# Kernel optimization log

Hardware: AMD Instinct MI355X
Metric: run time of the kernel (lower is better)

Reference implementation:

```python
import jax, jax.numpy as jnp
import numpy as np

B, S, D, H, HD = 8, 1374, 384, 6, 64
NUM_PATCHES = 1369  # (518 // 14) ** 2
NUM_PREFIX = 5      # 1 cls + 4 registers


def setup_inputs() -> dict:
    key = jax.random.key(0)
    ks = jax.random.split(key, 10)
    init = 0.02  # truncated_normal(0.02) approximated by scaled normal
    x = jax.random.normal(ks[0], (B, S, D), jnp.float32)
    wq = jax.random.truncated_normal(ks[1], -2.0, 2.0, (D, H, HD), jnp.float32) * init
    wk = jax.random.truncated_normal(ks[2], -2.0, 2.0, (D, H, HD), jnp.float32) * init
    wv = jax.random.truncated_normal(ks[3], -2.0, 2.0, (D, H, HD), jnp.float32) * init
    wo = jax.random.truncated_normal(ks[4], -2.0, 2.0, (H, HD, D), jnp.float32) * init
    bq = jnp.zeros((H, HD), jnp.float32)
    bk = jnp.zeros((H, HD), jnp.float32)
    bv = jnp.zeros((H, HD), jnp.float32)
    bo = jnp.zeros((D,), jnp.float32)
    keep_patch_indices = jax.random.randint(ks[5], (B, NUM_PATCHES), 0, NUM_PATCHES).astype(jnp.int64)
    return {"x": x, "wq": wq, "bq": bq, "wk": wk, "bk": bk, "wv": wv, "bv": bv,
            "wo": wo, "bo": bo, "keep_patch_indices": keep_patch_indices, "k_patches": 685}


def reference(x, wq, bq, wk, bk, wv, bv, wo, bo, keep_patch_indices, k_patches):
    # q/k/v projections: DenseGeneral to (heads, head_dim)
    q = jnp.einsum('bsd,dhe->bshe', x, wq) + bq
    k = jnp.einsum('bsd,dhe->bshe', x, wk) + bk
    v = jnp.einsum('bsd,dhe->bshe', x, wv) + bv

    z = jnp.einsum('bqhd,bkhd->bhqk', q / (HD ** 0.5), k)  # [B,H,S,S]
    attn_logits = z  # saved BEFORE masking (used by 'mse' criterion)

    # dynamic scatter mask: patch columns >= k_patches get -inf
    num_selected = keep_patch_indices.shape[1]
    patch_idx = jnp.arange(num_selected)
    indices_to_mask = jnp.where(patch_idx >= k_patches, patch_idx, num_selected) + NUM_PREFIX
    # out-of-bounds indices (== num_selected + NUM_PREFIX) are dropped by JAX scatter semantics
    z = z.at[:, :, :, indices_to_mask].set(-jnp.inf)

    attn_map = jax.nn.softmax(z, axis=-1)
    zo = jnp.einsum('bhqk,bkhd->bqhd', attn_map, v)
    output = jnp.einsum('bqhd,hdo->bqo', zo, wo) + bo  # wo contracts (heads, head_dim)

    # attn_aggregate = ['cls_token','reg_token','patch_token'], zoom_map_criterion='mse'
    am = attn_logits.mean(axis=1)  # mean over heads -> [B,S,S]
    aggs = jnp.stack([
        am[:, 0:1, :].mean(axis=1),      # cls token
        am[:, 1:5, :].mean(axis=1),      # register tokens
        am[:, 5:1374, :].mean(axis=1),   # patch tokens
    ], axis=1)                            # [B,3,S]
    attn_agg = aggs.mean(axis=1)          # [B,S]
    return output, attn_agg
```

## Files before the change

### kernel.cpp

```cpp
#include <hip/hip_runtime.h>
#include <stdint.h>

#define BB 8
#define SS 1374
#define DD 384
#define HH 6
#define HDIM 64
#define MROWS (BB*SS)
#define NPFX 5
#define SPAD 1376

typedef __attribute__((ext_vector_type(8))) short bf16x8;
typedef __attribute__((ext_vector_type(4))) float f32x4;
typedef __attribute__((ext_vector_type(2))) unsigned int u32x2;
typedef __attribute__((ext_vector_type(4))) unsigned int u32x4;
typedef u32x4 __attribute__((aligned(4))) u32x4_u;

__device__ __forceinline__ unsigned short f2bf(float f){
  union { float f; unsigned int u; } v; v.f = f;
  return (unsigned short)((v.u + 0x7FFFu + ((v.u >> 16) & 1u)) >> 16);
}
__device__ __forceinline__ float bf2f(unsigned short b){
  union { float f; unsigned int u; } v; v.u = ((unsigned int)b) << 16; return v.f;
}
__device__ __forceinline__ unsigned int pk_bf16(float a, float b){
#if __has_builtin(__builtin_amdgcn_cvt_pk_bf16_f32)
  typedef __attribute__((ext_vector_type(2))) __bf16 bfv2;
  bfv2 p = __builtin_amdgcn_cvt_pk_bf16_f32(a, b);
  union { bfv2 v; unsigned int u; } c; c.v = p; return c.u;
#else
  return (unsigned int)f2bf(a) | ((unsigned int)f2bf(b) << 16);
#endif
}

__global__ void k_prep_x(const float* __restrict__ x, unsigned short* __restrict__ xb,
                         float* __restrict__ xbar){
  int b = blockIdx.x / 43, ch = blockIdx.x % 43;
  int d = threadIdx.x;
  int s0 = ch*32, s1 = s0 + 32; if (s1 > SS) s1 = SS;
  float acc = 0.f;
  for (int s = s0; s < s1; ++s){
    float v = x[((size_t)b*SS + s)*DD + d];
    float w = (s == 0) ? (1.f/3.f) : (s < 5) ? (1.f/12.f) : (1.f/4107.f);
    acc += w * v;
    xb[((size_t)b*SS + s)*DD + d] = f2bf(v);
  }
  atomicAdd(&xbar[b*DD + d], acc);
}

__global__ void k_conv_w(const float* __restrict__ wq, const float* __restrict__ wk,
                         const float* __restrict__ wv, const float* __restrict__ wo,
                         unsigned short* __restrict__ wbT, unsigned short* __restrict__ woT){
  int i = blockIdx.x*blockDim.x + threadIdx.x;
  if (i < 1152*384){
    int n = i / 384, d = i % 384;
    const float* w = (n < 384) ? wq : (n < 768) ? wk : wv;
    wbT[i] = f2bf(w[(size_t)d*384 + (n % 384)]);
  } else if (i < 1152*384 + 384*384){
    int j = i - 1152*384;
    int n = j / 384, k = j % 384;
    woT[j] = f2bf(wo[(size_t)k*384 + n]);
  }
}

__global__ void k_qbar(const float* __restrict__ xbar, const float* __restrict__ wq,
                       const float* __restrict__ bq, float* __restrict__ qbar){
  __shared__ float xs[DD];
  int b = blockIdx.x, t = threadIdx.x;
  xs[t] = xbar[b*DD + t];
  __syncthreads();
  float acc = bq[t];
  for (int d = 0; d < DD; ++d) acc += xs[d]*wq[(size_t)d*384 + t];
  qbar[b*384 + t] = acc;
}

__global__ void k_agg(const float* __restrict__ qbar, const unsigned short* __restrict__ kg,
                      float* __restrict__ out_agg){
  __shared__ float qs[384];
  int b = blockIdx.x / 6, sb = blockIdx.x % 6;
  int t = threadIdx.x;
  for (int i = t; i < 384; i += 256) qs[i] = qbar[b*384 + i];
  __syncthreads();
  int s = sb*256 + t;
  if (s >= SS) return;
  float acc = 0.f;
  for (int h = 0; h < HH; ++h){
    const unsigned short* kr = kg + (((size_t)(b*HH + h))*SS + s)*64;
    const float* qh = qs + h*64;
    for (int c = 0; c < 8; ++c){
      u32x4 v = *(const u32x4*)(kr + c*8);
      #pragma unroll
      for (int j = 0; j < 4; ++j){
        unsigned int u = v[j];
        acc += qh[c*8 + 2*j]     * bf2f((unsigned short)(u & 0xFFFFu));
        acc += qh[c*8 + 2*j + 1] * bf2f((unsigned short)(u >> 16));
      }
    }
  }
  out_agg[b*SS + s] = acc * (1.f/48.f);
}

template<int MODE>
__global__ __launch_bounds__(256) void k_gemm(
    const unsigned short* __restrict__ A, const unsigned short* __restrict__ Bt,
    const float* __restrict__ b0, const float* __restrict__ b1, const float* __restrict__ b2,
    unsigned short* __restrict__ qg, unsigned short* __restrict__ kgp,
    unsigned short* __restrict__ vt, float* __restrict__ out)
{
  int mt = blockIdx.x % 86, nt = blockIdx.x / 86;
  const int t = threadIdx.x;
  const int w = t >> 6, lane = t & 63, quad = lane >> 4, l16 = lane & 15;
  const int wm = w >> 1, wn = w & 1;
  constexpr int SMEM_SH = (MODE==0) ? 13824 : 17408;
  __shared__ unsigned short smem[SMEM_SH];
  unsigned short* As = smem;
  unsigned short* Bs = smem + 9216;
  f32x4 acc[4][2];
  #pragma unroll
  for (int i=0;i<4;i++){ acc[i][0] = (f32x4){0,0,0,0}; acc[i][1] = (f32x4){0,0,0,0}; }
  const int m0 = mt*128, n0 = nt*64;

  const int ar = t >> 1, akb = (t & 1) * 32;
  int ga = m0 + ar; if (ga > MROWS-1) ga = MROWS-1;
  const unsigned short* ap = A + (size_t)ga*384 + akb;
  const int br = t >> 2, bkb = (t & 3) * 16;
  const unsigned short* bp = Bt + (size_t)(n0 + br)*384 + bkb;

  u32x4 ra[4], rb[2];
  #pragma unroll
  for (int i=0;i<4;i++) ra[i] = *(const u32x4*)(ap + i*8);
  rb[0] = *(const u32x4*)(bp); rb[1] = *(const u32x4*)(bp + 8);

  for (int kc = 0; kc < 6; ++kc){
    __syncthreads();
    #pragma unroll
    for (int i=0;i<4;i++) *(u32x4*)(As + ar*72 + akb + i*8) = ra[i];
    *(u32x4*)(Bs + br*72 + bkb)     = rb[0];
    *(u32x4*)(Bs + br*72 + bkb + 8) = rb[1];
    __syncthreads();
    if (kc + 1 < 6){
      int kn = (kc+1)*64;
      #pragma unroll
      for (int i=0;i<4;i++) ra[i] = *(const u32x4*)(ap + kn + i*8);
      rb[0] = *(const u32x4*)(bp + kn); rb[1] = *(const u32x4*)(bp + kn + 8);
    }
    #pragma unroll
    for (int kh = 0; kh < 2; ++kh){
      bf16x8 af[4], bfr[2];
      #pragma unroll
      for (int rf = 0; rf < 4; ++rf)
        af[rf] = *(const bf16x8*)(As + (wm*64 + rf*16 + l16)*72 + kh*32 + quad*8);
      #pragma unroll
      for (int cf = 0; cf < 2; ++cf)
        bfr[cf] = *(const bf16x8*)(Bs + (wn*32 + cf*16 + l16)*72 + kh*32 + quad*8);
      #pragma unroll
      for (int rf = 0; rf < 4; ++rf)
        #pragma unroll
        for (int cf = 0; cf < 2; ++cf)
          acc[rf][cf] = __builtin_amdgcn_mfma_f32_16x16x32_bf16(af[rf], bfr[cf], acc[rf][cf], 0,0,0);
    }
  }

  const int b0r = m0 / SS, s0r = m0 % SS;
  __syncthreads();
  if (MODE == 1){
    float* CsF = (float*)smem;
    #pragma unroll
    for (int cf = 0; cf < 2; ++cf){
      int e = wn*32 + cf*16 + l16;
      float bias = b0[n0 + e];
      #pragma unroll
      for (int rf = 0; rf < 4; ++rf){
        int rr = wm*64 + rf*16 + quad*4;
        #pragma unroll
        for (int r4 = 0; r4 < 4; ++r4)
          CsF[(rr + r4)*68 + e] = acc[rf][cf][r4] + bias;
      }
    }
    __syncthreads();
    #pragma unroll
    for (int p = 0; p < 8; ++p){
      int r = p*16 + (t >> 4), c = t & 15;
      int rr = m0 + r;
      if (rr < MROWS){
        f32x4 v = *(const f32x4*)(CsF + r*68 + c*4);
        *(f32x4*)(out + (size_t)rr*384 + n0 + c*4) = v;
      }
    }
  } else {
    const int mat = nt / 6, h = nt - mat*6;
    const float* bvp = (mat==0) ? b0 : (mat==1) ? b1 : b2;
    const float vsc = (mat==0) ? 0.125f : 1.f;
    if (mat < 2){
      unsigned short* Cs = As;
      unsigned short* dst = (mat==0) ? qg : kgp;
      #pragma unroll
      for (int cf = 0; cf < 2; ++cf){
        int e = wn*32 + cf*16 + l16;
        float bias = bvp[h*64 + e];
        #pragma unroll
        for (int rf = 0; rf < 4; ++rf){
          int rr = wm*64 + rf*16 + quad*4;
          #pragma unroll
          for (int r4 = 0; r4 < 4; ++r4)
            Cs[(rr + r4)*72 + e] = f2bf((acc[rf][cf][r4] + bias)*vsc);
        }
      }
      __syncthreads();
      #pragma unroll
      for (int p = 0; p < 4; ++p){
        int r = p*32 + (t >> 3), c = t & 7;
        int rr = m0 + r;
        if (rr < MROWS){
          int s = s0r + r, bb = b0r;
          if (s >= SS){ s -= SS; ++bb; }
          u32x4 v = *(const u32x4*)(Cs + r*72 + c*8);
          *(u32x4*)(dst + (((size_t)(bb*HH + h))*SS + s)*64 + c*8) = v;
        }
      }
    } else {
      unsigned short* CsV = As;
      #pragma unroll
      for (int cf = 0; cf < 2; ++cf){
        int e = wn*32 + cf*16 + l16;
        float bias = bvp[h*64 + e];
        #pragma unroll
        for (int rf = 0; rf < 4; ++rf){
          int rr = wm*64 + rf*16 + quad*4;
          #pragma unroll
          for (int p = 0; p < 2; ++p)
            *(unsigned int*)(CsV + e*136 + rr + p*2) =
                pk_bf16(acc[rf][cf][p*2] + bias, acc[rf][cf][p*2+1] + bias);
        }
      }
      __syncthreads();
      const bool nowrap = (s0r + 127 < SS) && (m0 + 127 < MROWS);
      if (nowrap){
        int e = t >> 2;
        unsigned short* vrow = vt + ((size_t)(b0r*HH + h)*64 + e)*SPAD + s0r;
        #pragma unroll
        for (int i = 0; i < 4; ++i){
          int c = (t & 3)*4 + i;
          u32x4 v = *(const u32x4*)(CsV + e*136 + c*8);
          *(u32x4_u*)(vrow + c*8) = v;
        }
      } else {
        for (int idx = t; idx < 64*64; idx += 256){
          int e = idx >> 6, sp = (idx & 63)*2;
          int rr = m0 + sp;
          if (rr < MROWS){
            int s = s0r + sp, bb = b0r;
            if (s >= SS){ s -= SS; ++bb; }
            *(unsigned int*)(vt + ((size_t)(bb*HH + h)*64 + e)*SPAD + s) =
                *(const unsigned int*)(CsV + e*136 + sp);
          }
        }
      }
    }
  }
}

__global__ __launch_bounds__(256) void k_attn(
    const unsigned short* __restrict__ qg, const unsigned short* __restrict__ kg,
    const unsigned short* __restrict__ vt, unsigned short* __restrict__ zo,
    const int* __restrict__ kpat)
{
  int t = threadIdx.x, w = t >> 6, lane = t & 63, quad = lane >> 4, l16 = lane & 15;
  int wid = blockIdx.x*4 + w;
  int bh = wid / 43, qt = wid - bh*43;
  int q0 = qt*32;
  int SK = NPFX + kpat[0]; if (SK > SS) SK = SS; if (SK < 1) SK = 1;
  int niter = (SK + 63) >> 6;
  __shared__ unsigned short Ps[4][32*72];
  unsigned short* Pw = &Ps[w][0];
  const unsigned short* kbase = kg + ((size_t)bh*SS)*64;
  const unsigned short* vbase = vt + ((size_t)bh*64)*SPAD;

  bf16x8 aq[2][2];
  #pragma unroll
  for (int qf = 0; qf < 2; ++qf){
    int qrow = q0 + qf*16 + l16; if (qrow > SS-1) qrow = SS-1;
    const unsigned short* p = qg + ((size_t)bh*SS + qrow)*64;
    aq[qf][0] = *(const bf16x8*)(p + quad*8);
    aq[qf][1] = *(const bf16x8*)(p + 32 + quad*8);
  }
  f32x4 o[2][4];
  #pragma unroll
  for (int qf=0;qf<2;qf++)
    #pragma unroll
    for (int nc=0;nc<4;nc++) o[qf][nc] = (f32x4){0.f,0.f,0.f,0.f};
  float rsum[2][4] = {{0.f,0.f,0.f,0.f},{0.f,0.f,0.f,0.f}};

  for (int it = 0; it < niter; ++it){
    int k0 = it*64;
    bool tail = (k0 + 64 > SK);
    #pragma unroll
    for (int ks = 0; ks < 2; ++ks){
      bf16x8 kf[2][2];
      #pragma unroll
      for (int ns = 0; ns < 2; ++ns){
        const unsigned short* kr = kbase + (size_t)(k0 + ks*32 + 2*l16 + ns)*64;
        kf[ns][0] = *(const bf16x8*)(kr + quad*8);
        kf[ns][1] = *(const bf16x8*)(kr + 32 + quad*8);
      }
      #pragma unroll
      for (int qf = 0; qf < 2; ++qf){
        float pp[2][4];
        #pragma unroll
        for (int ns = 0; ns < 2; ++ns){
          f32x4 zf = (f32x4){0.f,0.f,0.f,0.f};
          zf = __builtin_amdgcn_mfma_f32_16x16x32_bf16(aq[qf][0], kf[ns][0], zf, 0,0,0);
          zf = __builtin_amdgcn_mfma_f32_16x16x32_bf16(aq[qf][1], kf[ns][1], zf, 0,0,0);
          bool valid = !tail || (k0 + ks*32 + 2*l16 + ns) < SK;
          #pragma unroll
          for (int rg = 0; rg < 4; ++rg) pp[ns][rg] = valid ? __expf(zf[rg]) : 0.f;
        }
        #pragma unroll
        for (int rg = 0; rg < 4; ++rg){
          rsum[qf][rg] += pp[0][rg] + pp[1][rg];
          *(unsigned int*)(Pw + (qf*16 + quad*4 + rg)*72 + ks*32 + 2*l16) =
              pk_bf16(pp[0][rg], pp[1][rg]);
        }
      }
    }
    #pragma unroll
    for (int kc = 0; kc < 2; ++kc){
      bf16x8 ap0 = *(const bf16x8*)(Pw + l16*72        + kc*32 + quad*8);
      bf16x8 ap1 = *(const bf16x8*)(Pw + (16 + l16)*72 + kc*32 + quad*8);
      #pragma unroll
      for (int nc = 0; nc < 4; ++nc){
        bf16x8 vf = *(const bf16x8*)(vbase + (size_t)(nc*16 + l16)*SPAD + k0 + kc*32 + quad*8);
        o[0][nc] = __builtin_amdgcn_mfma_f32_16x16x32_bf16(ap0, vf, o[0][nc], 0,0,0);
        o[1][nc] = __builtin_amdgcn_mfma_f32_16x16x32_bf16(ap1, vf, o[1][nc], 0,0,0);
      }
    }
  }
  int b = bh / HH, h = bh - (bh/HH)*HH;
  #pragma unroll
  for (int qf = 0; qf < 2; ++qf){
    #pragma unroll
    for (int rg = 0; rg < 4; ++rg){
      float s = rsum[qf][rg];
      #pragma unroll
      for (int off = 8; off >= 1; off >>= 1) s += __shfl_xor(s, off);
      int q = q0 + qf*16 + quad*4 + rg;
      if (q >= SS) continue;
      float inv = 1.f / s;
      unsigned short* dst = zo + ((size_t)b*SS + q)*384 + h*64;
      #pragma unroll
      for (int nc = 0; nc < 4; ++nc) dst[nc*16 + l16] = f2bf(o[qf][nc][rg]*inv);
    }
  }
}

extern "C" void kernel_launch(void* const* d_in, const int* in_sizes, int n_in,
                              void* d_out, int out_size, void* d_ws, size_t ws_size,
                              hipStream_t stream){
  const float* x  = (const float*)d_in[0];
  const float* wq = (const float*)d_in[1];
  const float* bq = (const float*)d_in[2];
  const float* wk = (const float*)d_in[3];
  const float* bk = (const float*)d_in[4];
  const float* wv = (const float*)d_in[5];
  const float* bv = (const float*)d_in[6];
  const float* wo = (const float*)d_in[7];
  const float* bo = (const float*)d_in[8];
  const int* kpat = (const int*)d_in[10];
  float* out = (float*)d_out;
  float* out_agg = out + (size_t)MROWS*DD;

  char* ws = (char*)d_ws;
  unsigned short* xb  = (unsigned short*)(ws);
  unsigned short* wbT = (unsigned short*)(ws +  8441856);
  unsigned short* woT = (unsigned short*)(ws +  9326592);
  unsigned short* qg  = (unsigned short*)(ws +  9621504);
  unsigned short* kg  = (unsigned short*)(ws + 18063360);
  unsigned short* vt  = (unsigned short*)(ws + 26505216);
  unsigned short* zo  = (unsigned short*)(ws + 34959360);
  float* xbar         = (float*)(ws + 43401216);
  float* qbar         = (float*)(ws + 43413504);
  (void)in_sizes; (void)n_in; (void)out_size; (void)ws_size;

  hipMemsetAsync(xbar, 0, BB*DD*sizeof(float), stream);
  k_prep_x<<<BB*43, DD, 0, stream>>>(x, xb, xbar);
  k_conv_w<<<((1152*384 + 384*384) + 255)/256, 256, 0, stream>>>(wq, wk, wv, wo, wbT, woT);
  k_qbar<<<BB, DD, 0, stream>>>(xbar, wq, bq, qbar);
  k_gemm<0><<<86*18, 256, 0, stream>>>(xb, wbT, bq, bk, bv, qg, kg, vt, nullptr);
  k_attn<<<516, 256, 0, stream>>>(qg, kg, vt, zo, kpat);
  k_agg<<<BB*6, 256, 0, stream>>>(qbar, kg, out_agg);
  k_gemm<1><<<86*6, 256, 0, stream>>>(zo, woT, bo, nullptr, nullptr, nullptr, nullptr, nullptr, out);
}
```

Before: 208.8 us.

## Software-pipeline K/V loads in attention kernel and halve block size

The attention loop now double-buffers K fragments in registers, prefetching the next 64-key tile's K while the current one is computed, and loads all V fragments at the start of each iteration, ahead of the softmax/P work. Block size drops from 4 to 2 waves with twice as many blocks, which spreads the 2064 wave tasks over more CUs. The aim is to hide global-load latency behind MFMA and exp work. The cost is higher register pressure from the extra K and V buffers, which may lower occupancy.

```diff
diff --git a/kernel.cpp b/kernel.cpp
--- a/kernel.cpp
+++ b/kernel.cpp
@@ -260,18 +260,18 @@
   }
 }
 
-__global__ __launch_bounds__(256) void k_attn(
+__global__ __launch_bounds__(128) void k_attn(
     const unsigned short* __restrict__ qg, const unsigned short* __restrict__ kg,
     const unsigned short* __restrict__ vt, unsigned short* __restrict__ zo,
     const int* __restrict__ kpat)
 {
   int t = threadIdx.x, w = t >> 6, lane = t & 63, quad = lane >> 4, l16 = lane & 15;
-  int wid = blockIdx.x*4 + w;
+  int wid = blockIdx.x*2 + w;
   int bh = wid / 43, qt = wid - bh*43;
   int q0 = qt*32;
   int SK = NPFX + kpat[0]; if (SK > SS) SK = SS; if (SK < 1) SK = 1;
   int niter = (SK + 63) >> 6;
-  __shared__ unsigned short Ps[4][32*72];
+  __shared__ unsigned short Ps[2][32*72];
   unsigned short* Pw = &Ps[w][0];
   const unsigned short* kbase = kg + ((size_t)bh*SS)*64;
   const unsigned short* vbase = vt + ((size_t)bh*64)*SPAD;
@@ -291,26 +291,37 @@
     for (int nc=0;nc<4;nc++) o[qf][nc] = (f32x4){0.f,0.f,0.f,0.f};
   float rsum[2][4] = {{0.f,0.f,0.f,0.f},{0.f,0.f,0.f,0.f}};
 
-  for (int it = 0; it < niter; ++it){
-    int k0 = it*64;
-    bool tail = (k0 + 64 > SK);
-    #pragma unroll
-    for (int ks = 0; ks < 2; ++ks){
-      bf16x8 kf[2][2];
+  auto loadK = [&](int k0, bf16x8 (&kf)[2][2][2]){
+    #pragma unroll
+    for (int ks = 0; ks < 2; ++ks)
       #pragma unroll
       for (int ns = 0; ns < 2; ++ns){
         const unsigned short* kr = kbase + (size_t)(k0 + ks*32 + 2*l16 + ns)*64;
-        kf[ns][0] = *(const bf16x8*)(kr + quad*8);
-        kf[ns][1] = *(const bf16x8*)(kr + 32 + quad*8);
-      }
+        kf[ks][ns][0] = *(const bf16x8*)(kr + quad*8);
+        kf[ks][ns][1] = *(const bf16x8*)(kr + 32 + quad*8);
+      }
+  };
+
+  auto body = [&](int it, bf16x8 (&kfC)[2][2][2], bf16x8 (&kfN)[2][2][2]){
+    int k0 = it*64;
+    bf16x8 vf[2][4];
+    #pragma unroll
+    for (int kc = 0; kc < 2; ++kc)
+      #pragma unroll
+      for (int nc = 0; nc < 4; ++nc)
+        vf[kc][nc] = *(const bf16x8*)(vbase + (size_t)(nc*16 + l16)*SPAD + k0 + kc*32 + quad*8);
+    if (it + 1 < niter) loadK(k0 + 64, kfN);
+    bool tail = (k0 + 64 > SK);
+    #pragma unroll
+    for (int ks = 0; ks < 2; ++ks){
       #pragma unroll
       for (int qf = 0; qf < 2; ++qf){
         float pp[2][4];
         #pragma unroll
         for (int ns = 0; ns < 2; ++ns){
           f32x4 zf = (f32x4){0.f,0.f,0.f,0.f};
-          zf = __builtin_amdgcn_mfma_f32_16x16x32_bf16(aq[qf][0], kf[ns][0], zf, 0,0,0);
-          zf = __builtin_amdgcn_mfma_f32_16x16x32_bf16(aq[qf][1], kf[ns][1], zf, 0,0,0);
+          zf = __builtin_amdgcn_mfma_f32_16x16x32_bf16(aq[qf][0], kfC[ks][ns][0], zf, 0,0,0);
+          zf = __builtin_amdgcn_mfma_f32_16x16x32_bf16(aq[qf][1], kfC[ks][ns][1], zf, 0,0,0);
           bool valid = !tail || (k0 + ks*32 + 2*l16 + ns) < SK;
           #pragma unroll
           for (int rg = 0; rg < 4; ++rg) pp[ns][rg] = valid ? __expf(zf[rg]) : 0.f;
@@ -329,12 +340,19 @@
       bf16x8 ap1 = *(const bf16x8*)(Pw + (16 + l16)*72 + kc*32 + quad*8);
       #pragma unroll
       for (int nc = 0; nc < 4; ++nc){
-        bf16x8 vf = *(const bf16x8*)(vbase + (size_t)(nc*16 + l16)*SPAD + k0 + kc*32 + quad*8);
-        o[0][nc] = __builtin_amdgcn_mfma_f32_16x16x32_bf16(ap0, vf, o[0][nc], 0,0,0);
-        o[1][nc] = __builtin_amdgcn_mfma_f32_16x16x32_bf16(ap1, vf, o[1][nc], 0,0,0);
-      }
-    }
-  }
+        o[0][nc] = __builtin_amdgcn_mfma_f32_16x16x32_bf16(ap0, vf[kc][nc], o[0][nc], 0,0,0);
+        o[1][nc] = __builtin_amdgcn_mfma_f32_16x16x32_bf16(ap1, vf[kc][nc], o[1][nc], 0,0,0);
+      }
+    }
+  };
+
+  bf16x8 kfA[2][2][2], kfB[2][2][2];
+  loadK(0, kfA);
+  for (int it = 0; it < niter; it += 2){
+    body(it, kfA, kfB);
+    if (it + 1 < niter) body(it + 1, kfB, kfA);
+  }
+
   int b = bh / HH, h = bh - (bh/HH)*HH;
   #pragma unroll
   for (int qf = 0; qf < 2; ++qf){
@@ -386,7 +404,7 @@
   k_conv_w<<<((1152*384 + 384*384) + 255)/256, 256, 0, stream>>>(wq, wk, wv, wo, wbT, woT);
   k_qbar<<<BB, DD, 0, stream>>>(xbar, wq, bq, qbar);
   k_gemm<0><<<86*18, 256, 0, stream>>>(xb, wbT, bq, bk, bv, qg, kg, vt, nullptr);
-  k_attn<<<516, 256, 0, stream>>>(qg, kg, vt, zo, kpat);
+  k_attn<<<1032, 128, 0, stream>>>(qg, kg, vt, zo, kpat);
   k_agg<<<BB*6, 256, 0, stream>>>(qbar, kg, out_agg);
   k_gemm<1><<<86*6, 256, 0, stream>>>(zo, woT, bo, nullptr, nullptr, nullptr, nullptr, nullptr, out);
 }
```

After: 198.3 us. 1.05x faster.

## Stage K/V tiles in shared memory with register prefetch in attention kernel

Applied to the files above, without the earlier changes.

The attention kernel now uses 128-thread blocks of two waves, each owning 16 query rows. The block cooperatively loads each 64-key K and V tile into LDS, with the next tile prefetched into registers while the current one is computed. Before, each wave read K and V straight from global memory. The goal is to share K/V loads across waves and hide global latency with more, smaller blocks. The cost is two barriers per iteration and less query reuse per wave: 16 rows instead of 32.

```diff
diff --git a/kernel.cpp b/kernel.cpp
--- a/kernel.cpp
+++ b/kernel.cpp
@@ -260,96 +260,106 @@
   }
 }
 
-__global__ __launch_bounds__(256) void k_attn(
+#define KSTR 72
+__global__ __launch_bounds__(128) void k_attn(
     const unsigned short* __restrict__ qg, const unsigned short* __restrict__ kg,
     const unsigned short* __restrict__ vt, unsigned short* __restrict__ zo,
     const int* __restrict__ kpat)
 {
+  const int QB = 43;
+  int qb = blockIdx.x % QB, bh = blockIdx.x / QB;
   int t = threadIdx.x, w = t >> 6, lane = t & 63, quad = lane >> 4, l16 = lane & 15;
-  int wid = blockIdx.x*4 + w;
-  int bh = wid / 43, qt = wid - bh*43;
-  int q0 = qt*32;
   int SK = NPFX + kpat[0]; if (SK > SS) SK = SS; if (SK < 1) SK = 1;
   int niter = (SK + 63) >> 6;
-  __shared__ unsigned short Ps[4][32*72];
+  __shared__ unsigned short Ks[64*KSTR];
+  __shared__ unsigned short Vs[64*KSTR];
+  __shared__ unsigned short Ps[2][16*KSTR];
   unsigned short* Pw = &Ps[w][0];
+  int q0 = qb*32 + w*16;
+  bf16x8 aq[2];
+  {
+    int qrow = q0 + l16; if (qrow > SS-1) qrow = SS-1;
+    const unsigned short* p = qg + ((size_t)bh*SS + qrow)*64;
+    aq[0] = *(const bf16x8*)(p + quad*8);
+    aq[1] = *(const bf16x8*)(p + 32 + quad*8);
+  }
+  f32x4 o[4];
+  #pragma unroll
+  for (int i=0;i<4;i++) o[i] = (f32x4){0.f,0.f,0.f,0.f};
+  float rsum[4] = {0.f,0.f,0.f,0.f};
+
+  const int srow = t >> 1, shalf = (t & 1)*32;
   const unsigned short* kbase = kg + ((size_t)bh*SS)*64;
   const unsigned short* vbase = vt + ((size_t)bh*64)*SPAD;
-
-  bf16x8 aq[2][2];
+  u32x4 rk[4], rv[4];
   #pragma unroll
-  for (int qf = 0; qf < 2; ++qf){
-    int qrow = q0 + qf*16 + l16; if (qrow > SS-1) qrow = SS-1;
-    const unsigned short* p = qg + ((size_t)bh*SS + qrow)*64;
-    aq[qf][0] = *(const bf16x8*)(p + quad*8);
-    aq[qf][1] = *(const bf16x8*)(p + 32 + quad*8);
-  }
-  f32x4 o[2][4];
-  #pragma unroll
-  for (int qf=0;qf<2;qf++)
-    #pragma unroll
-    for (int nc=0;nc<4;nc++) o[qf][nc] = (f32x4){0.f,0.f,0.f,0.f};
-  float rsum[2][4] = {{0.f,0.f,0.f,0.f},{0.f,0.f,0.f,0.f}};
+  for (int i=0;i<4;i++){
+    rk[i] = *(const u32x4*)(kbase + (size_t)srow*64 + shalf + i*8);
+    rv[i] = *(const u32x4*)(vbase + (size_t)srow*SPAD + shalf + i*8);
+  }
 
   for (int it = 0; it < niter; ++it){
     int k0 = it*64;
+    __syncthreads();
+    #pragma unroll
+    for (int i=0;i<4;i++){
+      *(u32x4*)(Ks + srow*KSTR + shalf + i*8) = rk[i];
+      *(u32x4*)(Vs + srow*KSTR + shalf + i*8) = rv[i];
+    }
+    __syncthreads();
+    if (it + 1 < niter){
+      int kn = k0 + 64;
+      #pragma unroll
+      for (int i=0;i<4;i++){
+        rk[i] = *(const u32x4*)(kbase + (size_t)(kn + srow)*64 + shalf + i*8);
+        rv[i] = *(const u32x4*)(vbase + (size_t)srow*SPAD + kn + shalf + i*8);
+      }
+    }
     bool tail = (k0 + 64 > SK);
     #pragma unroll
     for (int ks = 0; ks < 2; ++ks){
-      bf16x8 kf[2][2];
+      float pp[2][4];
       #pragma unroll
       for (int ns = 0; ns < 2; ++ns){
-        const unsigned short* kr = kbase + (size_t)(k0 + ks*32 + 2*l16 + ns)*64;
-        kf[ns][0] = *(const bf16x8*)(kr + quad*8);
-        kf[ns][1] = *(const bf16x8*)(kr + 32 + quad*8);
-      }
-      #pragma unroll
-      for (int qf = 0; qf < 2; ++qf){
-        float pp[2][4];
-        #pragma unroll
-        for (int ns = 0; ns < 2; ++ns){
-          f32x4 zf = (f32x4){0.f,0.f,0.f,0.f};
-          zf = __builtin_amdgcn_mfma_f32_16x16x32_bf16(aq[qf][0], kf[ns][0], zf, 0,0,0);
-          zf = __builtin_amdgcn_mfma_f32_16x16x32_bf16(aq[qf][1], kf[ns][1], zf, 0,0,0);
-          bool valid = !tail || (k0 + ks*32 + 2*l16 + ns) < SK;
-          #pragma unroll
-          for (int rg = 0; rg < 4; ++rg) pp[ns][rg] = valid ? __expf(zf[rg]) : 0.f;
-        }
-        #pragma unroll
-        for (int rg = 0; rg < 4; ++rg){
-          rsum[qf][rg] += pp[0][rg] + pp[1][rg];
-          *(unsigned int*)(Pw + (qf*16 + quad*4 + rg)*72 + ks*32 + 2*l16) =
-              pk_bf16(pp[0][rg], pp[1][rg]);
-        }
+        f32x4 zf = (f32x4){0.f,0.f,0.f,0.f};
+        #pragma unroll
+        for (int ec = 0; ec < 2; ++ec){
+          bf16x8 bkf = *(const bf16x8*)(Ks + (ks*32 + 2*l16 + ns)*KSTR + ec*32 + quad*8);
+          zf = __builtin_amdgcn_mfma_f32_16x16x32_bf16(aq[ec], bkf, zf, 0,0,0);
+        }
+        bool valid = !tail || (k0 + ks*32 + 2*l16 + ns) < SK;
+        #pragma unroll
+        for (int rg = 0; rg < 4; ++rg) pp[ns][rg] = valid ? __expf(zf[rg]) : 0.f;
+      }
+      #pragma unroll
+      for (int rg = 0; rg < 4; ++rg){
+        rsum[rg] += pp[0][rg] + pp[1][rg];
+        *(unsigned int*)(Pw + (quad*4 + rg)*KSTR + ks*32 + 2*l16) =
+            pk_bf16(pp[0][rg], pp[1][rg]);
       }
     }
     #pragma unroll
     for (int kc = 0; kc < 2; ++kc){
-      bf16x8 ap0 = *(const bf16x8*)(Pw + l16*72        + kc*32 + quad*8);
-      bf16x8 ap1 = *(const bf16x8*)(Pw + (16 + l16)*72 + kc*32 + quad*8);
+      bf16x8 ap = *(const bf16x8*)(Pw + l16*KSTR + kc*32 + quad*8);
       #pragma unroll
       for (int nc = 0; nc < 4; ++nc){
-        bf16x8 vf = *(const bf16x8*)(vbase + (size_t)(nc*16 + l16)*SPAD + k0 + kc*32 + quad*8);
-        o[0][nc] = __builtin_amdgcn_mfma_f32_16x16x32_bf16(ap0, vf, o[0][nc], 0,0,0);
-        o[1][nc] = __builtin_amdgcn_mfma_f32_16x16x32_bf16(ap1, vf, o[1][nc], 0,0,0);
+        bf16x8 vf = *(const bf16x8*)(Vs + (nc*16 + l16)*KSTR + kc*32 + quad*8);
+        o[nc] = __builtin_amdgcn_mfma_f32_16x16x32_bf16(ap, vf, o[nc], 0,0,0);
       }
     }
   }
   int b = bh / HH, h = bh - (bh/HH)*HH;
   #pragma unroll
-  for (int qf = 0; qf < 2; ++qf){
-    #pragma unroll
-    for (int rg = 0; rg < 4; ++rg){
-      float s = rsum[qf][rg];
-      #pragma unroll
-      for (int off = 8; off >= 1; off >>= 1) s += __shfl_xor(s, off);
-      int q = q0 + qf*16 + quad*4 + rg;
-      if (q >= SS) continue;
-      float inv = 1.f / s;
-      unsigned short* dst = zo + ((size_t)b*SS + q)*384 + h*64;
-      #pragma unroll
-      for (int nc = 0; nc < 4; ++nc) dst[nc*16 + l16] = f2bf(o[qf][nc][rg]*inv);
-    }
+  for (int rg = 0; rg < 4; ++rg){
+    float s = rsum[rg];
+    #pragma unroll
+    for (int off = 8; off >= 1; off >>= 1) s += __shfl_xor(s, off);
+    int q = q0 + quad*4 + rg;
+    if (q >= SS) continue;
+    float inv = 1.f / s;
+    unsigned short* dst = zo + ((size_t)b*SS + q)*384 + h*64;
+    #pragma unroll
+    for (int nc = 0; nc < 4; ++nc) dst[nc*16 + l16] = f2bf(o[nc][rg]*inv);
   }
 }
 
@@ -386,7 +396,7 @@
   k_conv_w<<<((1152*384 + 384*384) + 255)/256, 256, 0, stream>>>(wq, wk, wv, wo, wbT, woT);
   k_qbar<<<BB, DD, 0, stream>>>(xbar, wq, bq, qbar);
   k_gemm<0><<<86*18, 256, 0, stream>>>(xb, wbT, bq, bk, bv, qg, kg, vt, nullptr);
-  k_attn<<<516, 256, 0, stream>>>(qg, kg, vt, zo, kpat);
+  k_attn<<<48*43, 128, 0, stream>>>(qg, kg, vt, zo, kpat);
   k_agg<<<BB*6, 256, 0, stream>>>(qbar, kg, out_agg);
   k_gemm<1><<<86*6, 256, 0, stream>>>(zo, woT, bo, nullptr, nullptr, nullptr, nullptr, nullptr, out);
 }
```

New measurement: 191.6 us. 1.09x faster.

## Keep attention probabilities in registers via transposed MFMA, prefetch K tiles

Applied to the files above, without the earlier changes.

Computes S^T = K·Q^T with MFMA so each lane's probability outputs already sit in the B-operand layout for the P·V MFMA. This removes the per-wave LDS round trip for P. It also double-buffers K fragments across 32-key iterations and writes the output as packed vector stores. Register pressure rises from the two K buffers and the V fragments held per iteration.

```diff
diff --git a/kernel.cpp b/kernel.cpp
--- a/kernel.cpp
+++ b/kernel.cpp
@@ -270,9 +270,7 @@
   int bh = wid / 43, qt = wid - bh*43;
   int q0 = qt*32;
   int SK = NPFX + kpat[0]; if (SK > SS) SK = SS; if (SK < 1) SK = 1;
-  int niter = (SK + 63) >> 6;
-  __shared__ unsigned short Ps[4][32*72];
-  unsigned short* Pw = &Ps[w][0];
+  int niter = (SK + 31) >> 5;
   const unsigned short* kbase = kg + ((size_t)bh*SS)*64;
   const unsigned short* vbase = vt + ((size_t)bh*64)*SPAD;
 
@@ -289,66 +287,81 @@
   for (int qf=0;qf<2;qf++)
     #pragma unroll
     for (int nc=0;nc<4;nc++) o[qf][nc] = (f32x4){0.f,0.f,0.f,0.f};
-  float rsum[2][4] = {{0.f,0.f,0.f,0.f},{0.f,0.f,0.f,0.f}};
-
-  for (int it = 0; it < niter; ++it){
-    int k0 = it*64;
-    bool tail = (k0 + 64 > SK);
-    #pragma unroll
-    for (int ks = 0; ks < 2; ++ks){
-      bf16x8 kf[2][2];
-      #pragma unroll
-      for (int ns = 0; ns < 2; ++ns){
-        const unsigned short* kr = kbase + (size_t)(k0 + ks*32 + 2*l16 + ns)*64;
-        kf[ns][0] = *(const bf16x8*)(kr + quad*8);
-        kf[ns][1] = *(const bf16x8*)(kr + 32 + quad*8);
-      }
-      #pragma unroll
-      for (int qf = 0; qf < 2; ++qf){
-        float pp[2][4];
-        #pragma unroll
-        for (int ns = 0; ns < 2; ++ns){
-          f32x4 zf = (f32x4){0.f,0.f,0.f,0.f};
-          zf = __builtin_amdgcn_mfma_f32_16x16x32_bf16(aq[qf][0], kf[ns][0], zf, 0,0,0);
-          zf = __builtin_amdgcn_mfma_f32_16x16x32_bf16(aq[qf][1], kf[ns][1], zf, 0,0,0);
-          bool valid = !tail || (k0 + ks*32 + 2*l16 + ns) < SK;
-          #pragma unroll
-          for (int rg = 0; rg < 4; ++rg) pp[ns][rg] = valid ? __expf(zf[rg]) : 0.f;
-        }
+  float rsum[2] = {0.f, 0.f};
+
+  const int krow_off = ((l16 >> 2) << 3) + (l16 & 3);
+  auto loadK = [&](int k0, bf16x8 (&kf)[2][2]){
+    #pragma unroll
+    for (int s = 0; s < 2; ++s){
+      const unsigned short* kr = kbase + (size_t)(k0 + krow_off + s*4)*64;
+      kf[s][0] = *(const bf16x8*)(kr + quad*8);
+      kf[s][1] = *(const bf16x8*)(kr + 32 + quad*8);
+    }
+  };
+
+  auto body = [&](int it, bf16x8 (&kfC)[2][2], bf16x8 (&kfN)[2][2]){
+    int k0 = it*32;
+    bf16x8 vf[4];
+    #pragma unroll
+    for (int nc = 0; nc < 4; ++nc)
+      vf[nc] = *(const bf16x8*)(vbase + (size_t)(nc*16 + l16)*SPAD + k0 + quad*8);
+    if (it + 1 < niter) loadK(k0 + 32, kfN);
+    bool tail = (k0 + 32 > SK);
+    int kidx0 = k0 + quad*8;
+    float ps[2][2][4];
+    #pragma unroll
+    for (int qf = 0; qf < 2; ++qf){
+      #pragma unroll
+      for (int s = 0; s < 2; ++s){
+        f32x4 zf = (f32x4){0.f,0.f,0.f,0.f};
+        zf = __builtin_amdgcn_mfma_f32_16x16x32_bf16(kfC[s][0], aq[qf][0], zf, 0,0,0);
+        zf = __builtin_amdgcn_mfma_f32_16x16x32_bf16(kfC[s][1], aq[qf][1], zf, 0,0,0);
         #pragma unroll
         for (int rg = 0; rg < 4; ++rg){
-          rsum[qf][rg] += pp[0][rg] + pp[1][rg];
-          *(unsigned int*)(Pw + (qf*16 + quad*4 + rg)*72 + ks*32 + 2*l16) =
-              pk_bf16(pp[0][rg], pp[1][rg]);
-        }
-      }
-    }
-    #pragma unroll
-    for (int kc = 0; kc < 2; ++kc){
-      bf16x8 ap0 = *(const bf16x8*)(Pw + l16*72        + kc*32 + quad*8);
-      bf16x8 ap1 = *(const bf16x8*)(Pw + (16 + l16)*72 + kc*32 + quad*8);
-      #pragma unroll
-      for (int nc = 0; nc < 4; ++nc){
-        bf16x8 vf = *(const bf16x8*)(vbase + (size_t)(nc*16 + l16)*SPAD + k0 + kc*32 + quad*8);
-        o[0][nc] = __builtin_amdgcn_mfma_f32_16x16x32_bf16(ap0, vf, o[0][nc], 0,0,0);
-        o[1][nc] = __builtin_amdgcn_mfma_f32_16x16x32_bf16(ap1, vf, o[1][nc], 0,0,0);
-      }
-    }
-  }
+          bool valid = !tail || (kidx0 + s*4 + rg) < SK;
+          float p = valid ? __expf(zf[rg]) : 0.f;
+          ps[qf][s][rg] = p;
+          rsum[qf] += p;
+        }
+      }
+    }
+    #pragma unroll
+    for (int qf = 0; qf < 2; ++qf){
+      u32x4 pu;
+      pu[0] = pk_bf16(ps[qf][0][0], ps[qf][0][1]);
+      pu[1] = pk_bf16(ps[qf][0][2], ps[qf][0][3]);
+      pu[2] = pk_bf16(ps[qf][1][0], ps[qf][1][1]);
+      pu[3] = pk_bf16(ps[qf][1][2], ps[qf][1][3]);
+      union { u32x4 u; bf16x8 b; } cv; cv.u = pu;
+      #pragma unroll
+      for (int nc = 0; nc < 4; ++nc)
+        o[qf][nc] = __builtin_amdgcn_mfma_f32_16x16x32_bf16(vf[nc], cv.b, o[qf][nc], 0,0,0);
+    }
+  };
+
+  bf16x8 kfA[2][2], kfB[2][2];
+  loadK(0, kfA);
+  for (int it = 0; it < niter; it += 2){
+    body(it, kfA, kfB);
+    if (it + 1 < niter) body(it + 1, kfB, kfA);
+  }
+
   int b = bh / HH, h = bh - (bh/HH)*HH;
   #pragma unroll
   for (int qf = 0; qf < 2; ++qf){
-    #pragma unroll
-    for (int rg = 0; rg < 4; ++rg){
-      float s = rsum[qf][rg];
-      #pragma unroll
-      for (int off = 8; off >= 1; off >>= 1) s += __shfl_xor(s, off);
-      int q = q0 + qf*16 + quad*4 + rg;
-      if (q >= SS) continue;
-      float inv = 1.f / s;
-      unsigned short* dst = zo + ((size_t)b*SS + q)*384 + h*64;
-      #pragma unroll
-      for (int nc = 0; nc < 4; ++nc) dst[nc*16 + l16] = f2bf(o[qf][nc][rg]*inv);
+    float s = rsum[qf];
+    s += __shfl_xor(s, 16);
+    s += __shfl_xor(s, 32);
+    int q = q0 + qf*16 + l16;
+    if (q >= SS) continue;
+    float inv = 1.f / s;
+    unsigned short* dst = zo + ((size_t)b*SS + q)*384 + h*64;
+    #pragma unroll
+    for (int nc = 0; nc < 4; ++nc){
+      u32x2 ov;
+      ov[0] = pk_bf16(o[qf][nc][0]*inv, o[qf][nc][1]*inv);
+      ov[1] = pk_bf16(o[qf][nc][2]*inv, o[qf][nc][3]*inv);
+      *(u32x2*)(dst + nc*16 + quad*4) = ov;
     }
   }
 }
```

Result: faster. 204.1 us (-2.2%).
